# Kernel optimization log

Measured on AMD Instinct MI355X. Metric: run time of the kernel, lower is better.

The kernel has to match this reference:

```python
import jax, jax.numpy as jnp
import numpy as np

B, S, N, IN_DIM = 64, 12, 170, 1
E, L, C, H, OUT = 128, 4, 2, 8, 1
OFFSET, PAD = 0, 1          # seq_offset=0 -> Conv2d padding (0,1)
LOOKUP, MAXLEN = 0, 100
EPS = 1e-5


def _shift(x, s):
    """y[:, i] = x[:, i+s] along axis 1, zero padded."""
    if s == 0:
        return x
    z = jnp.zeros_like(x[:, :abs(s)])
    if s > 0:
        return jnp.concatenate([x[:, s:], z], axis=1)
    return jnp.concatenate([z, x[:, :s]], axis=1)


def _masked_conv_diag(x, w):
    """Diagonal of Conv2d(kernel=(1,3), pad=(0,PAD)) applied to the causally
    masked repeated tensor, computed directly without the O(B*S*S*E) blowup:
      out[b,i] = sum_k W[:,:,k] @ (mask(i, i+k-PAD) * x[b, i+k-PAD])
    where mask(i,j) = (j <= i) or (j < OFFSET)."""
    i = jnp.arange(x.shape[1])
    out = None
    for k in range(3):
        s = k - PAD
        term = jnp.einsum('bse,oe->bso', _shift(x, s), w[:, :, k])
        if s > 0:  # only future taps can be masked out
            term = term * (i + s < OFFSET).astype(x.dtype)[None, :, None]
        out = term if out is None else out + term
    return out


def _conv1d_k3(x, w, b):
    """Conv1d over the seq dim, kernel 3, padding 1, with bias. x:[b,s,e]."""
    out = b
    for k in range(3):
        out = out + jnp.einsum('bse,oe->bso', _shift(x, k - 1), w[:, :, k])
    return out


def _layer_norm(x, g, b):
    m = jnp.mean(x, -1, keepdims=True)
    v = jnp.mean((x - m) ** 2, -1, keepdims=True)
    return (x - m) * jax.lax.rsqrt(v + EPS) * g + b


def _mha(q_in, kv_in, w, b, mask=None):
    dh = E // H
    q = (q_in @ w[0] + b[0]).reshape(q_in.shape[0], q_in.shape[1], H, dh)
    k = (kv_in @ w[1] + b[1]).reshape(kv_in.shape[0], kv_in.shape[1], H, dh)
    v = (kv_in @ w[2] + b[2]).reshape(kv_in.shape[0], kv_in.shape[1], H, dh)
    s = jnp.einsum('bqhd,bkhd->bhqk', q, k) * np.float32(1.0 / np.sqrt(dh))
    if mask is not None:
        s = jnp.where(mask[None, None], s, jnp.float32(-1e9))
    a = jax.nn.softmax(s, axis=-1)
    o = jnp.einsum('bhqk,bkhd->bqhd', a, v).reshape(q_in.shape[0], q_in.shape[1], E)
    return o @ w[3] + b[3]


def setup_inputs() -> dict:
    key = jax.random.key(0)
    ks = jax.random.split(key, 16)

    def nrm(k, shape, scale=0.05):
        return scale * jax.random.normal(k, shape, dtype=jnp.float32)

    # sinusoidal positional table, length MAXLEN
    pos = np.arange(MAXLEN)[:, None].astype(np.float32)
    div = np.exp(-np.log(10000.0) * np.arange(0, E, 2) / E).astype(np.float32)
    pe = np.zeros((MAXLEN, E), np.float32)
    pe[:, 0::2] = np.sin(pos * div)
    pe[:, 1::2] = np.cos(pos * div)

    return {
        'x': jax.random.normal(ks[0], (B, S, N, IN_DIM), jnp.float32),
        'enc_x': jax.random.normal(ks[1], (C, B * N, S, E), jnp.float32),
        'tgt_mask': jnp.tril(jnp.ones((S, S), bool)),
        'emb_w': nrm(ks[2], (IN_DIM, E), 1.0),
        'emb_b': jnp.zeros((E,), jnp.float32),
        'pe': jnp.asarray(pe),
        'conv_q_w': nrm(ks[3], (L, E, E, 3)),
        'conv_k_w': nrm(ks[4], (L, C, E, E, 3)),
        'conv_k_b': jnp.zeros((L, C, E), jnp.float32),
        'sa_w': nrm(ks[5], (L, 4, E, E)),
        'sa_b': jnp.zeros((L, 4, E), jnp.float32),
        'ca_w': nrm(ks[6], (L, C, 4, E, E)),
        'ca_b': jnp.zeros((L, C, 4, E), jnp.float32),
        'ff_w1': nrm(ks[7], (L, E, 4 * E)),
        'ff_b1': jnp.zeros((L, 4 * E), jnp.float32),
        'ff_w2': nrm(ks[8], (L, 4 * E, E)),
        'ff_b2': jnp.zeros((L, E), jnp.float32),
        'ln_g': jnp.ones((L, 3, E), jnp.float32),
        'ln_b': jnp.zeros((L, 3, E), jnp.float32),
        'fc_w': nrm(ks[9], (E, OUT)),
        'fc_b': jnp.zeros((OUT,), jnp.float32),
    }


def reference(x, enc_x, tgt_mask, emb_w, emb_b, pe, conv_q_w, conv_k_w, conv_k_b,
              sa_w, sa_b, ca_w, ca_b, ff_w1, ff_b1, ff_w2, ff_b2, ln_g, ln_b,
              fc_w, fc_b):
    h = x @ emb_w + emb_b                                    # [B,S,N,E]
    h = jnp.transpose(h, (1, 0, 2, 3)).reshape(S, B * N, E)  # [S,B*N,E]
    h = jnp.transpose(h, (1, 0, 2))                          # [B*N,S,E]
    h = h + pe[LOOKUP:LOOKUP + S]
    for l in range(L):
        # local trends: causal masked-conv query (the fused diagonal)
        h = _masked_conv_diag(h, conv_q_w[l])
        enc_list = [_conv1d_k3(enc_x[i], conv_k_w[l, i], conv_k_b[l, i])
                    for i in range(C)]
        # decoder block: self-attn -> cross-attn (avg over features) -> FFN
        h = _layer_norm(h + _mha(h, h, sa_w[l], sa_b[l], tgt_mask),
                        ln_g[l, 0], ln_b[l, 0])
        cross = sum(_mha(h, enc_list[i], ca_w[l, i], ca_b[l, i])
                    for i in range(C)) / C
        h = _layer_norm(h + cross, ln_g[l, 1], ln_b[l, 1])
        f = jax.nn.relu(h @ ff_w1[l] + ff_b1[l]) @ ff_w2[l] + ff_b2[l]
        h = _layer_norm(h + f, ln_g[l, 2], ln_b[l, 2])
    out = h @ fc_w + fc_b                                    # [B*N,S,OUT]
    out = jnp.transpose(out, (1, 0, 2)).reshape(S, B, N, OUT)
    return jnp.transpose(out, (1, 0, 2, 3))                  # [B,S,N,OUT]
```

## Files before the change

kernel.cpp:

```cpp
#include <hip/hip_runtime.h>


#define B_   64
#define S_   12
#define N_   170
#define BN_  (B_*N_)
#define E_   128
#define L_   4
#define C_   2
#define H_   8
#define DH_  16
#define FF_  512
#define EPS_ 1e-5f
#define THREADS 512

typedef unsigned short u16;
typedef __attribute__((ext_vector_type(4))) float f32x4;
typedef __attribute__((ext_vector_type(8))) u16   us8;
typedef __attribute__((ext_vector_type(4))) u16   us4;
typedef __attribute__((ext_vector_type(8))) __bf16 bf16x8;
union FragU { us8 u; bf16x8 b; };

__device__ __forceinline__ u16 f2bf(float f) {
    __bf16 h = (__bf16)f;
    return __builtin_bit_cast(u16, h);
}
__device__ __forceinline__ float bf2f(u16 s) {
    return __builtin_bit_cast(float, (unsigned)s << 16);
}

__global__ void k_wpack(const float* __restrict__ cq, const float* __restrict__ sa,
                        const float* __restrict__ ck, const float* __restrict__ ca,
                        const float* __restrict__ f1, const float* __restrict__ f2,
                        u16* __restrict__ wp) {
    int f  = blockIdx.x * 256 + threadIdx.x;
    int l  = f / 57344, fl = f % 57344;
    const float* src; int sk, so, KS, q;
    if (fl < 4096)        { int tap = fl >> 11; q = fl & 2047; KS = 4;
                            src = cq + (size_t)l*49152 + tap;            sk = 3;   so = 384; }
    else if (fl < 12288)  { int j = (fl - 4096) >> 11; q = fl & 2047; KS = 4;
                            src = sa + (size_t)(l*4 + j)*16384;          sk = 128; so = 1;   }
    else if (fl < 24576)  { int ct = (fl - 12288) >> 11; q = fl & 2047; KS = 4;
                            int ci = ct / 3, tap = ct % 3;
                            src = ck + (size_t)(l*2 + ci)*49152 + tap;   sk = 3;   so = 384; }
    else if (fl < 40960)  { int cj = (fl - 24576) >> 11; q = fl & 2047; KS = 4;
                            src = ca + (size_t)(l*8 + cj)*16384;         sk = 128; so = 1;   }
    else if (fl < 49152)  { q = fl - 40960; KS = 4;
                            src = f1 + (size_t)l*65536;                  sk = 512; so = 1;   }
    else                  { q = fl - 49152; KS = 16;
                            src = f2 + (size_t)l*65536;                  sk = 128; so = 1;   }
    int lane = q & 63, tt = q >> 6;
    int ks = tt % KS, ntile = tt / KS;
    int k0 = ks*32 + ((lane >> 4) << 3);
    int o  = ntile*16 + (lane & 15);
    us8 w;
    #pragma unroll
    for (int i = 0; i < 8; i++) w[i] = f2bf(src[(size_t)(k0 + i)*sk + (size_t)o*so]);
    *(us8*)(wp + (size_t)f*8) = w;
}

__device__ __forceinline__ void stage48(const float* __restrict__ src, u16* dst, int t) {
    for (int i = t; i < 1536; i += THREADS) {
        const f32x4 v = ((const f32x4*)src)[i];
        int elem = i << 2;
        int row = elem >> 7, colb = (elem & 127) << 1;
        us4 w; w[0] = f2bf(v[0]); w[1] = f2bf(v[1]); w[2] = f2bf(v[2]); w[3] = f2bf(v[3]);
        *(us4*)((char*)dst + (((row << 8) + colb) ^ ((row & 7) << 4))) = w;
    }
}

__device__ __forceinline__ void stage48_embed(const float* __restrict__ x,
    const float* __restrict__ ew, const float* __restrict__ eb,
    const float* __restrict__ pe, int bn0, u16* dst, int t) {
    for (int i = t; i < 1536; i += THREADS) {
        int elem = i << 2;
        int row = elem >> 7, col = elem & 127;
        int g = row / 12, s = row - g*12;
        int bn = bn0 + g, b = bn / N_, n = bn - b*N_;
        float xv = x[(b*S_ + s)*N_ + n];
        const f32x4 w  = *(const f32x4*)(ew + col);
        const f32x4 bb = *(const f32x4*)(eb + col);
        const f32x4 p  = *(const f32x4*)(pe + s*E_ + col);
        us4 o; o[0] = f2bf(xv*w[0] + bb[0] + p[0]); o[1] = f2bf(xv*w[1] + bb[1] + p[1]);
               o[2] = f2bf(xv*w[2] + bb[2] + p[2]); o[3] = f2bf(xv*w[3] + bb[3] + p[3]);
        *(us4*)((char*)dst + (((row << 8) + (col << 1)) ^ ((row & 7) << 4))) = o;
    }
}

__device__ __forceinline__ void acc_init(f32x4 (&acc)[3], const float* bias, int wave, int lane) {
    float bv = bias ? bias[wave*16 + (lane & 15)] : 0.f;
    #pragma unroll
    for (int mt = 0; mt < 3; mt++) {
        acc[mt][0] = bv; acc[mt][1] = bv; acc[mt][2] = bv; acc[mt][3] = bv;
    }
}

__device__ __forceinline__ bf16x8 ldA(const u16* A, int row, int colb) {
    FragU fu; fu.u = *(const us8*)((const char*)A + (((row << 8) + colb) ^ ((row & 7) << 4)));
    return fu.b;
}

template<int KSTOT>
__device__ __forceinline__ void gemm48(const u16* A, const us8* __restrict__ WP, int ksOff,
                                       f32x4 (&acc)[3], int wave, int lane) {
    #pragma unroll
    for (int ks = 0; ks < 4; ks++) {
        int colb = (ks*32 + ((lane >> 4) << 3)) << 1;
        bf16x8 a[3];
        #pragma unroll
        for (int mt = 0; mt < 3; mt++) a[mt] = ldA(A, mt*16 + (lane & 15), colb);
        FragU fb; fb.u = WP[(wave*KSTOT + ksOff + ks)*64 + lane];
        #pragma unroll
        for (int mt = 0; mt < 3; mt++)
            acc[mt] = __builtin_amdgcn_mfma_f32_16x16x32_bf16(a[mt], fb.b, acc[mt], 0, 0, 0);
    }
}

__device__ __forceinline__ void gemm48_x3(const u16* A,
        const us8* __restrict__ B0, const us8* __restrict__ B1, const us8* __restrict__ B2,
        f32x4 (&c0)[3], f32x4 (&c1)[3], f32x4 (&c2)[3], int wave, int lane) {
    #pragma unroll
    for (int ks = 0; ks < 4; ks++) {
        int colb = (ks*32 + ((lane >> 4) << 3)) << 1;
        bf16x8 a[3];
        #pragma unroll
        for (int mt = 0; mt < 3; mt++) a[mt] = ldA(A, mt*16 + (lane & 15), colb);
        FragU f0, f1, f2;
        int bi = (wave*4 + ks)*64 + lane;
        f0.u = B0[bi]; f1.u = B1[bi]; f2.u = B2[bi];
        #pragma unroll
        for (int mt = 0; mt < 3; mt++) {
            c0[mt] = __builtin_amdgcn_mfma_f32_16x16x32_bf16(a[mt], f0.b, c0[mt], 0, 0, 0);
            c1[mt] = __builtin_amdgcn_mfma_f32_16x16x32_bf16(a[mt], f1.b, c1[mt], 0, 0, 0);
            c2[mt] = __builtin_amdgcn_mfma_f32_16x16x32_bf16(a[mt], f2.b, c2[mt], 0, 0, 0);
        }
    }
}

__device__ __forceinline__ void gemm48_x2(const u16* A,
        const us8* __restrict__ B0, const us8* __restrict__ B1,
        f32x4 (&c0)[3], f32x4 (&c1)[3], int wave, int lane) {
    #pragma unroll
    for (int ks = 0; ks < 4; ks++) {
        int colb = (ks*32 + ((lane >> 4) << 3)) << 1;
        bf16x8 a[3];
        #pragma unroll
        for (int mt = 0; mt < 3; mt++) a[mt] = ldA(A, mt*16 + (lane & 15), colb);
        FragU f0, f1;
        int bi = (wave*4 + ks)*64 + lane;
        f0.u = B0[bi]; f1.u = B1[bi];
        #pragma unroll
        for (int mt = 0; mt < 3; mt++) {
            c0[mt] = __builtin_amdgcn_mfma_f32_16x16x32_bf16(a[mt], f0.b, c0[mt], 0, 0, 0);
            c1[mt] = __builtin_amdgcn_mfma_f32_16x16x32_bf16(a[mt], f1.b, c1[mt], 0, 0, 0);
        }
    }
}

__device__ __forceinline__ void gemm48_rows(const u16* A, const u16* ZR, const int (&sr)[3],
                                            const us8* __restrict__ WP,
                                            f32x4 (&acc)[3], int wave, int lane) {
    #pragma unroll
    for (int ks = 0; ks < 4; ks++) {
        int colb = (ks*32 + ((lane >> 4) << 3)) << 1;
        bf16x8 a[3];
        #pragma unroll
        for (int mt = 0; mt < 3; mt++) {
            const char* p = (sr[mt] >= 0)
                ? (const char*)A + (((sr[mt] << 8) + colb) ^ ((sr[mt] & 7) << 4))
                : (const char*)ZR + colb;
            FragU fu; fu.u = *(const us8*)p;
            a[mt] = fu.b;
        }
        FragU fb; fb.u = WP[(wave*4 + ks)*64 + lane];
        #pragma unroll
        for (int mt = 0; mt < 3; mt++)
            acc[mt] = __builtin_amdgcn_mfma_f32_16x16x32_bf16(a[mt], fb.b, acc[mt], 0, 0, 0);
    }
}

template<bool RELU>
__device__ __forceinline__ void acc_store_bf(const f32x4 (&acc)[3], u16* Bp, int wave, int lane) {
    #pragma unroll
    for (int mt = 0; mt < 3; mt++)
    #pragma unroll
    for (int r = 0; r < 4; r++) {
        int row = mt*16 + ((lane >> 4) << 2) + r;
        int col = wave*16 + (lane & 15);
        float v = acc[mt][r];
        if (RELU) v = fmaxf(v, 0.f);
        *(u16*)((char*)Bp + (((row << 8) + (col << 1)) ^ ((row & 7) << 4))) = f2bf(v);
    }
}

__device__ __forceinline__ void ld16(const u16* Bf, int row, int colb, float* o16) {
    int x = (row & 7) << 4;
    int base = (row << 8) + colb;
    us8 u0 = *(const us8*)((const char*)Bf + (base ^ x));
    us8 u1 = *(const us8*)((const char*)Bf + ((base + 16) ^ x));
    #pragma unroll
    for (int d = 0; d < 8; d++) { o16[d] = bf2f(u0[d]); o16[8+d] = bf2f(u1[d]); }
}

template<bool MASK>
__device__ __forceinline__ void attn48(u16* QA, const u16* KB, const u16* VB, int t) {
    if (t < 384) {
        int g = t / 96, rem = t % 96;
        int hh = rem / 12, qi = rem % 12;
        int hb2 = hh << 5;
        int rq = g*12 + qi;
        float qv[16]; ld16(QA, rq, hb2, qv);
        float sc[12]; float mx = -1e30f;
        #pragma unroll
        for (int j = 0; j < 12; j++) {
            float kv[16]; ld16(KB, g*12 + j, hb2, kv);
            float s = 0.f;
            #pragma unroll
            for (int d = 0; d < 16; d++) s += qv[d]*kv[d];
            s *= 0.25f;
            if (MASK && j > qi) s = -1e30f;
            sc[j] = s; mx = fmaxf(mx, s);
        }
        float sum = 0.f;
        #pragma unroll
        for (int j = 0; j < 12; j++) { sc[j] = __expf(sc[j] - mx); sum += sc[j]; }
        float inv = 1.f/sum;
        float ov[16];
        #pragma unroll
        for (int d = 0; d < 16; d++) ov[d] = 0.f;
        #pragma unroll
        for (int j = 0; j < 12; j++) {
            float vv[16]; ld16(VB, g*12 + j, hb2, vv);
            #pragma unroll
            for (int d = 0; d < 16; d++) ov[d] += sc[j]*vv[d];
        }
        int x = (rq & 7) << 4;
        us8 w0, w1;
        #pragma unroll
        for (int d = 0; d < 8; d++) { w0[d] = f2bf(ov[d]*inv); w1[d] = f2bf(ov[8+d]*inv); }
        *(us8*)((char*)QA + (((rq << 8) + hb2) ^ x))      = w0;
        *(us8*)((char*)QA + (((rq << 8) + hb2 + 16) ^ x)) = w1;
    }
}

__device__ __forceinline__ void ln_inreg(f32x4 (&v)[3], float* lnbuf,
                                         const float* __restrict__ g, const float* __restrict__ bb,
                                         int wave, int lane) {
    int col = wave*16 + (lane & 15);
    float gc = g[col], bc = bb[col];
    #pragma unroll
    for (int mt = 0; mt < 3; mt++)
    #pragma unroll
    for (int r = 0; r < 4; r++) {
        float a = v[mt][r];
        float p = a, q = a*a;
        #pragma unroll
        for (int off = 1; off < 16; off <<= 1) { p += __shfl_xor(p, off); q += __shfl_xor(q, off); }
        if ((lane & 15) == 0) {
            int row = mt*16 + ((lane >> 4) << 2) + r;
            lnbuf[(row*8 + wave)*2]     = p;
            lnbuf[(row*8 + wave)*2 + 1] = q;
        }
    }
    __syncthreads();
    #pragma unroll
    for (int mt = 0; mt < 3; mt++)
    #pragma unroll
    for (int r = 0; r < 4; r++) {
        int row = mt*16 + ((lane >> 4) << 2) + r;
        float sum = 0.f, ss = 0.f;
        #pragma unroll
        for (int w2 = 0; w2 < 8; w2++) { sum += lnbuf[(row*8 + w2)*2]; ss += lnbuf[(row*8 + w2)*2 + 1]; }
        float m   = sum * (1.f/128.f);
        float var = ss * (1.f/128.f) - m*m;
        float inv = rsqrtf(var + EPS_);
        v[mt][r] = (v[mt][r] - m)*inv*gc + bc;
    }
}

template<bool EMB, bool FIN>
__global__ void __launch_bounds__(THREADS, 2)
k_layer(float* __restrict__ h, const float* __restrict__ x,
        const float* __restrict__ ew, const float* __restrict__ ebp, const float* __restrict__ pe,
        const float* __restrict__ encx, const u16* __restrict__ lw,
        const float* __restrict__ sab, const float* __restrict__ ckb, const float* __restrict__ cab,
        const float* __restrict__ fb1, const float* __restrict__ fb2,
        const float* __restrict__ lg, const float* __restrict__ lb,
        const float* __restrict__ fcw, const float* __restrict__ fcb,
        float* __restrict__ outp) {
    __shared__ __align__(16) u16 P0[6144], P1[6144], P2[6144], P3[6144], P4[6144], ZR[128];
    __shared__ __align__(16) float lnbuf[48*8*2];

    int t = threadIdx.x, wave = t >> 6, lane = t & 63;
    int bid = blockIdx.x;
    float* hp = h + (size_t)bid * (48*128);

    if (t < 64) ((unsigned*)ZR)[t] = 0;
    if (EMB) stage48_embed(x, ew, ebp, pe, bid*4, P0, t);
    else     stage48(hp, P0, t);
    stage48(encx + (size_t)(bid*4) * (S_*E_), P4, t);
    __syncthreads();

    int gg[3], rr[3];
    #pragma unroll
    for (int mt = 0; mt < 3; mt++) { int m = mt*16 + (lane & 15); gg[mt] = m/12; rr[mt] = m - gg[mt]*12; }

    f32x4 cacc[3];
    acc_init(cacc, nullptr, wave, lane);
    {
        int sr[3];
        #pragma unroll
        for (int mt = 0; mt < 3; mt++) { int r2 = rr[mt] - 1; sr[mt] = (r2 >= 0) ? gg[mt]*12 + r2 : -1; }
        gemm48_rows(P0, ZR, sr, (const us8*)lw, cacc, wave, lane);
        #pragma unroll
        for (int mt = 0; mt < 3; mt++) sr[mt] = gg[mt]*12 + rr[mt];
        gemm48_rows(P0, ZR, sr, (const us8*)(lw + 16384), cacc, wave, lane);
    }
    acc_store_bf<false>(cacc, P1, wave, lane);
    __syncthreads();

    {
        const us8* sap = (const us8*)(lw + 32768);
        f32x4 aq[3], ak[3], av[3];
        acc_init(aq, sab,       wave, lane);
        acc_init(ak, sab + 128, wave, lane);
        acc_init(av, sab + 256, wave, lane);
        gemm48_x3(P1, sap, sap + 2048, sap + 4096, aq, ak, av, wave, lane);
        acc_store_bf<false>(aq, P0, wave, lane);
        acc_store_bf<false>(ak, P2, wave, lane);
        acc_store_bf<false>(av, P3, wave, lane);
    }
    __syncthreads();
    attn48<true>(P0, P2, P3, t);
    __syncthreads();

    f32x4 hres[3];
    {
        f32x4 a[3];
        acc_init(a, sab + 384, wave, lane);
        gemm48<4>(P0, (const us8*)(lw + 81920), 0, a, wave, lane);
        #pragma unroll
        for (int mt = 0; mt < 3; mt++) hres[mt] = a[mt] + cacc[mt];
    }
    ln_inreg(hres, lnbuf, lg, lb, wave, lane);
    acc_store_bf<false>(hres, P1, wave, lane);
    __syncthreads();

    f32x4 creg[3];
    {
        int col = wave*16 + (lane & 15);
        float bv = cab[3*128 + col] + cab[7*128 + col];
        #pragma unroll
        for (int mt = 0; mt < 3; mt++) { creg[mt][0]=bv; creg[mt][1]=bv; creg[mt][2]=bv; creg[mt][3]=bv; }
    }
    int srf[3], srp[3], srn[3];
    #pragma unroll
    for (int mt = 0; mt < 3; mt++) {
        int r2 = rr[mt] - 1; srp[mt] = (r2 >= 0) ? gg[mt]*12 + r2 : -1;
        srf[mt] = gg[mt]*12 + rr[mt];
        r2 = rr[mt] + 1;     srn[mt] = (r2 < 12) ? gg[mt]*12 + r2 : -1;
    }

    {
        const us8* ckp = (const us8*)(lw + 98304);
        f32x4 a[3];
        acc_init(a, ckb, wave, lane);
        gemm48_rows(P4, ZR, srp, ckp,        a, wave, lane);
        gemm48_rows(P4, ZR, srf, ckp + 2048, a, wave, lane);
        gemm48_rows(P4, ZR, srn, ckp + 4096, a, wave, lane);
        acc_store_bf<false>(a, P3, wave, lane);
    }
    __syncthreads();
    const us8* cap0 = (const us8*)(lw + 196608);
    {
        f32x4 aq[3], ak[3], av[3];
        acc_init(aq, cab,           wave, lane);
        gemm48<4>(P1, cap0, 0, aq, wave, lane);
        acc_store_bf<false>(aq, P0, wave, lane);
        acc_init(ak, cab + 128, wave, lane);
        acc_init(av, cab + 256, wave, lane);
        gemm48_x2(P3, cap0 + 2048, cap0 + 4096, ak, av, wave, lane);
        acc_store_bf<false>(ak, P2, wave, lane);
        acc_store_bf<false>(av, P4, wave, lane);
    }
    __syncthreads();
    stage48(encx + ((size_t)BN_ + bid*4) * (S_*E_), P3, t);
    attn48<false>(P0, P2, P4, t);
    __syncthreads();
    gemm48<4>(P0, cap0 + 6144, 0, creg, wave, lane);
    __syncthreads();

    {
        const us8* ckp = (const us8*)(lw + 98304 + 3*16384);
        f32x4 a[3];
        acc_init(a, ckb + 128, wave, lane);
        gemm48_rows(P3, ZR, srp, ckp,        a, wave, lane);
        gemm48_rows(P3, ZR, srf, ckp + 2048, a, wave, lane);
        gemm48_rows(P3, ZR, srn, ckp + 4096, a, wave, lane);
        acc_store_bf<false>(a, P0, wave, lane);
    }
    __syncthreads();
    const us8* cap1 = (const us8*)(lw + 196608 + 4*16384);
    {
        f32x4 aq[3], ak[3], av[3];
        acc_init(aq, cab + 4*128, wave, lane);
        gemm48<4>(P1, cap1, 0, aq, wave, lane);
        acc_store_bf<false>(aq, P2, wave, lane);
        acc_init(ak, cab + 5*128, wave, lane);
        acc_init(av, cab + 6*128, wave, lane);
        gemm48_x2(P0, cap1 + 2048, cap1 + 4096, ak, av, wave, lane);
        acc_store_bf<false>(ak, P3, wave, lane);
        acc_store_bf<false>(av, P4, wave, lane);
    }
    __syncthreads();
    attn48<false>(P2, P3, P4, t);
    __syncthreads();
    gemm48<4>(P2, cap1 + 6144, 0, creg, wave, lane);

    #pragma unroll
    for (int mt = 0; mt < 3; mt++) hres[mt] = hres[mt] + 0.5f*creg[mt];
    __syncthreads();
    ln_inreg(hres, lnbuf, lg + 128, lb + 128, wave, lane);
    acc_store_bf<false>(hres, P1, wave, lane);
    __syncthreads();

    f32x4 ffacc[3];
    acc_init(ffacc, fb2, wave, lane);
    #pragma unroll
    for (int c = 0; c < 4; c++) {
        u16* MB = (c & 1) ? P3 : P2;
        {
            f32x4 a[3];
            acc_init(a, fb1 + c*128, wave, lane);
            gemm48<4>(P1, (const us8*)(lw + 327680) + c*2048, 0, a, wave, lane);
            acc_store_bf<true>(a, MB, wave, lane);
        }
        __syncthreads();
        gemm48<16>(MB, (const us8*)(lw + 393216), c*4, ffacc, wave, lane);
    }
    #pragma unroll
    for (int mt = 0; mt < 3; mt++) hres[mt] = hres[mt] + ffacc[mt];
    ln_inreg(hres, lnbuf, lg + 256, lb + 256, wave, lane);

    if (FIN) {
        float fw = fcw[wave*16 + (lane & 15)];
        float pr[3][4];
        #pragma unroll
        for (int mt = 0; mt < 3; mt++)
        #pragma unroll
        for (int r = 0; r < 4; r++) {
            float p = hres[mt][r]*fw;
            #pragma unroll
            for (int off = 1; off < 16; off <<= 1) p += __shfl_xor(p, off);
            pr[mt][r] = p;
        }
        __syncthreads();
        if ((lane & 15) == 0) {
            #pragma unroll
            for (int mt = 0; mt < 3; mt++)
            #pragma unroll
            for (int r = 0; r < 4; r++) {
                int row = mt*16 + ((lane >> 4) << 2) + r;
                lnbuf[row*8 + wave] = pr[mt][r];
            }
        }
        __syncthreads();
        if (t < 48) {
            float s8 = fcb[0];
            #pragma unroll
            for (int w2 = 0; w2 < 8; w2++) s8 += lnbuf[t*8 + w2];
            int bn = bid*4 + t/12, s = t % 12;
            int b = bn / N_, n = bn - b*N_;
            outp[(b*S_ + s)*N_ + n] = s8;
        }
    } else {
        #pragma unroll
        for (int mt = 0; mt < 3; mt++)
        #pragma unroll
        for (int r = 0; r < 4; r++) {
            int row = mt*16 + ((lane >> 4) << 2) + r;
            int col = wave*16 + (lane & 15);
            hp[row*128 + col] = hres[mt][r];
        }
    }
}

extern "C" void kernel_launch(void* const* d_in, const int* in_sizes, int n_in,
                              void* d_out, int out_size, void* d_ws, size_t ws_size,
                              hipStream_t stream) {
    const float* x        = (const float*)d_in[0];
    const float* enc_x    = (const float*)d_in[1];
    const float* emb_w    = (const float*)d_in[3];
    const float* emb_b    = (const float*)d_in[4];
    const float* pe       = (const float*)d_in[5];
    const float* conv_q_w = (const float*)d_in[6];
    const float* conv_k_w = (const float*)d_in[7];
    const float* conv_k_b = (const float*)d_in[8];
    const float* sa_w     = (const float*)d_in[9];
    const float* sa_b     = (const float*)d_in[10];
    const float* ca_w     = (const float*)d_in[11];
    const float* ca_b     = (const float*)d_in[12];
    const float* ff_w1    = (const float*)d_in[13];
    const float* ff_b1    = (const float*)d_in[14];
    const float* ff_w2    = (const float*)d_in[15];
    const float* ff_b2    = (const float*)d_in[16];
    const float* ln_g     = (const float*)d_in[17];
    const float* ln_b     = (const float*)d_in[18];
    const float* fc_w     = (const float*)d_in[19];
    const float* fc_b     = (const float*)d_in[20];

    const size_t HN = (size_t)BN_ * S_ * E_;
    float* h  = (float*)d_ws;
    u16* wpk  = (u16*)((float*)d_ws + HN);

    k_wpack<<<896, 256, 0, stream>>>(conv_q_w, sa_w, conv_k_w, ca_w, ff_w1, ff_w2, wpk);

    for (int l = 0; l < L_; l++) {
        const u16* lw = wpk + (size_t)l*458752;
        const float* sab = sa_b + l*512;
        const float* ckb = conv_k_b + l*256;
        const float* cab = ca_b + l*1024;
        const float* fb1 = ff_b1 + l*512;
        const float* fb2 = ff_b2 + l*128;
        const float* lg  = ln_g + l*384;
        const float* lb  = ln_b + l*384;
        if (l == 0)
            k_layer<true, false><<<BN_/4, THREADS, 0, stream>>>(h, x, emb_w, emb_b, pe, enc_x, lw,
                sab, ckb, cab, fb1, fb2, lg, lb, fc_w, fc_b, (float*)d_out);
        else if (l == L_-1)
            k_layer<false, true><<<BN_/4, THREADS, 0, stream>>>(h, x, emb_w, emb_b, pe, enc_x, lw,
                sab, ckb, cab, fb1, fb2, lg, lb, fc_w, fc_b, (float*)d_out);
        else
            k_layer<false, false><<<BN_/4, THREADS, 0, stream>>>(h, x, emb_w, emb_b, pe, enc_x, lw,
                sab, ckb, cab, fb1, fb2, lg, lb, fc_w, fc_b, (float*)d_out);
    }
}
```

Baseline: 1.832 ms.

## Shrink per-block tile to two sequences with padded 16-row groups and 2x2 wave tiles

Each block now handles 2 sequences (24 rows) instead of 4 (48 rows), using 256 threads. Each sequence is padded to 16 rows so every MFMA M-tile lines up with one sequence, and each wave computes a 2x2 block of 16x16 tiles instead of a 3x1 strip. The intent is to cut shared memory per block, raise occupancy, reuse each weight fragment across two M-tiles and simplify the conv row indexing. In exchange, 4 of every 16 rows are padding, so a quarter of the MFMA work is spent on unused rows, and each weight fragment is reused across fewer rows.

```diff
diff --git a/kernel.cpp b/kernel.cpp
--- a/kernel.cpp
+++ b/kernel.cpp
@@ -12,7 +12,7 @@
 #define DH_  16
 #define FF_  512
 #define EPS_ 1e-5f
-#define THREADS 512
+#define THREADS 256
 
 typedef unsigned short u16;
 typedef __attribute__((ext_vector_type(4))) float f32x4;
@@ -59,23 +59,32 @@
     *(us8*)(wp + (size_t)f*8) = w;
 }
 
-__device__ __forceinline__ void stage48(const float* __restrict__ src, u16* dst, int t) {
-    for (int i = t; i < 1536; i += THREADS) {
+__device__ __forceinline__ void stage24(const float* __restrict__ src, u16* dst, int t) {
+    #pragma unroll
+    for (int it = 0; it < 3; it++) {
+        int i = t + it*THREADS;
         const f32x4 v = ((const f32x4*)src)[i];
         int elem = i << 2;
-        int row = elem >> 7, colb = (elem & 127) << 1;
+        int srow = elem >> 7;
+        int g = srow / 12, s = srow - g*12;
+        int row = g*16 + s;
+        int colb = (elem & 127) << 1;
         us4 w; w[0] = f2bf(v[0]); w[1] = f2bf(v[1]); w[2] = f2bf(v[2]); w[3] = f2bf(v[3]);
         *(us4*)((char*)dst + (((row << 8) + colb) ^ ((row & 7) << 4))) = w;
     }
 }
 
-__device__ __forceinline__ void stage48_embed(const float* __restrict__ x,
+__device__ __forceinline__ void stage24_embed(const float* __restrict__ x,
     const float* __restrict__ ew, const float* __restrict__ eb,
     const float* __restrict__ pe, int bn0, u16* dst, int t) {
-    for (int i = t; i < 1536; i += THREADS) {
+    #pragma unroll
+    for (int it = 0; it < 3; it++) {
+        int i = t + it*THREADS;
         int elem = i << 2;
-        int row = elem >> 7, col = elem & 127;
-        int g = row / 12, s = row - g*12;
+        int srow = elem >> 7;
+        int g = srow / 12, s = srow - g*12;
+        int row = g*16 + s;
+        int col = elem & 127;
         int bn = bn0 + g, b = bn / N_, n = bn - b*N_;
         float xv = x[(b*S_ + s)*N_ + n];
         const f32x4 w  = *(const f32x4*)(ew + col);
@@ -87,11 +96,14 @@
     }
 }
 
-__device__ __forceinline__ void acc_init(f32x4 (&acc)[3], const float* bias, int wave, int lane) {
-    float bv = bias ? bias[wave*16 + (lane & 15)] : 0.f;
-    #pragma unroll
-    for (int mt = 0; mt < 3; mt++) {
-        acc[mt][0] = bv; acc[mt][1] = bv; acc[mt][2] = bv; acc[mt][3] = bv;
+__device__ __forceinline__ void acc_init(f32x4 (&acc)[2][2], const float* bias, int wave, int lane) {
+    #pragma unroll
+    for (int nt = 0; nt < 2; nt++) {
+        float bv = bias ? bias[(wave*2 + nt)*16 + (lane & 15)] : 0.f;
+        #pragma unroll
+        for (int mt = 0; mt < 2; mt++) {
+            acc[mt][nt][0] = bv; acc[mt][nt][1] = bv; acc[mt][nt][2] = bv; acc[mt][nt][3] = bv;
+        }
     }
 }
 
@@ -101,93 +113,105 @@
 }
 
 template<int KSTOT>
-__device__ __forceinline__ void gemm48(const u16* A, const us8* __restrict__ WP, int ksOff,
-                                       f32x4 (&acc)[3], int wave, int lane) {
+__device__ __forceinline__ void gemm24(const u16* A, const us8* __restrict__ WP, int ksOff,
+                                       f32x4 (&acc)[2][2], int wave, int lane) {
     #pragma unroll
     for (int ks = 0; ks < 4; ks++) {
         int colb = (ks*32 + ((lane >> 4) << 3)) << 1;
-        bf16x8 a[3];
-        #pragma unroll
-        for (int mt = 0; mt < 3; mt++) a[mt] = ldA(A, mt*16 + (lane & 15), colb);
-        FragU fb; fb.u = WP[(wave*KSTOT + ksOff + ks)*64 + lane];
-        #pragma unroll
-        for (int mt = 0; mt < 3; mt++)
-            acc[mt] = __builtin_amdgcn_mfma_f32_16x16x32_bf16(a[mt], fb.b, acc[mt], 0, 0, 0);
-    }
-}
-
-__device__ __forceinline__ void gemm48_x3(const u16* A,
-        const us8* __restrict__ B0, const us8* __restrict__ B1, const us8* __restrict__ B2,
-        f32x4 (&c0)[3], f32x4 (&c1)[3], f32x4 (&c2)[3], int wave, int lane) {
+        bf16x8 a[2];
+        #pragma unroll
+        for (int mt = 0; mt < 2; mt++) a[mt] = ldA(A, mt*16 + (lane & 15), colb);
+        #pragma unroll
+        for (int nt = 0; nt < 2; nt++) {
+            FragU fb; fb.u = WP[((wave*2 + nt)*KSTOT + ksOff + ks)*64 + lane];
+            #pragma unroll
+            for (int mt = 0; mt < 2; mt++)
+                acc[mt][nt] = __builtin_amdgcn_mfma_f32_16x16x32_bf16(a[mt], fb.b, acc[mt][nt], 0, 0, 0);
+        }
+    }
+}
+
+__device__ __forceinline__ void gemm24_rows(const u16* A, const u16* ZR, const int (&sr)[2],
+                                            const us8* __restrict__ WP,
+                                            f32x4 (&acc)[2][2], int wave, int lane) {
     #pragma unroll
     for (int ks = 0; ks < 4; ks++) {
         int colb = (ks*32 + ((lane >> 4) << 3)) << 1;
-        bf16x8 a[3];
-        #pragma unroll
-        for (int mt = 0; mt < 3; mt++) a[mt] = ldA(A, mt*16 + (lane & 15), colb);
-        FragU f0, f1, f2;
-        int bi = (wave*4 + ks)*64 + lane;
-        f0.u = B0[bi]; f1.u = B1[bi]; f2.u = B2[bi];
-        #pragma unroll
-        for (int mt = 0; mt < 3; mt++) {
-            c0[mt] = __builtin_amdgcn_mfma_f32_16x16x32_bf16(a[mt], f0.b, c0[mt], 0, 0, 0);
-            c1[mt] = __builtin_amdgcn_mfma_f32_16x16x32_bf16(a[mt], f1.b, c1[mt], 0, 0, 0);
-            c2[mt] = __builtin_amdgcn_mfma_f32_16x16x32_bf16(a[mt], f2.b, c2[mt], 0, 0, 0);
-        }
-    }
-}
-
-__device__ __forceinline__ void gemm48_x2(const u16* A,
-        const us8* __restrict__ B0, const us8* __restrict__ B1,
-        f32x4 (&c0)[3], f32x4 (&c1)[3], int wave, int lane) {
-    #pragma unroll
-    for (int ks = 0; ks < 4; ks++) {
-        int colb = (ks*32 + ((lane >> 4) << 3)) << 1;
-        bf16x8 a[3];
-        #pragma unroll
-        for (int mt = 0; mt < 3; mt++) a[mt] = ldA(A, mt*16 + (lane & 15), colb);
-        FragU f0, f1;
-        int bi = (wave*4 + ks)*64 + lane;
-        f0.u = B0[bi]; f1.u = B1[bi];
-        #pragma unroll
-        for (int mt = 0; mt < 3; mt++) {
-            c0[mt] = __builtin_amdgcn_mfma_f32_16x16x32_bf16(a[mt], f0.b, c0[mt], 0, 0, 0);
-            c1[mt] = __builtin_amdgcn_mfma_f32_16x16x32_bf16(a[mt], f1.b, c1[mt], 0, 0, 0);
-        }
-    }
-}
-
-__device__ __forceinline__ void gemm48_rows(const u16* A, const u16* ZR, const int (&sr)[3],
-                                            const us8* __restrict__ WP,
-                                            f32x4 (&acc)[3], int wave, int lane) {
-    #pragma unroll
-    for (int ks = 0; ks < 4; ks++) {
-        int colb = (ks*32 + ((lane >> 4) << 3)) << 1;
-        bf16x8 a[3];
-        #pragma unroll
-        for (int mt = 0; mt < 3; mt++) {
+        bf16x8 a[2];
+        #pragma unroll
+        for (int mt = 0; mt < 2; mt++) {
             const char* p = (sr[mt] >= 0)
                 ? (const char*)A + (((sr[mt] << 8) + colb) ^ ((sr[mt] & 7) << 4))
                 : (const char*)ZR + colb;
             FragU fu; fu.u = *(const us8*)p;
             a[mt] = fu.b;
         }
-        FragU fb; fb.u = WP[(wave*4 + ks)*64 + lane];
-        #pragma unroll
-        for (int mt = 0; mt < 3; mt++)
-            acc[mt] = __builtin_amdgcn_mfma_f32_16x16x32_bf16(a[mt], fb.b, acc[mt], 0, 0, 0);
+        #pragma unroll
+        for (int nt = 0; nt < 2; nt++) {
+            FragU fb; fb.u = WP[((wave*2 + nt)*4 + ks)*64 + lane];
+            #pragma unroll
+            for (int mt = 0; mt < 2; mt++)
+                acc[mt][nt] = __builtin_amdgcn_mfma_f32_16x16x32_bf16(a[mt], fb.b, acc[mt][nt], 0, 0, 0);
+        }
+    }
+}
+
+__device__ __forceinline__ void gemm24_x3(const u16* A,
+        const us8* __restrict__ B0, const us8* __restrict__ B1, const us8* __restrict__ B2,
+        f32x4 (&c0)[2][2], f32x4 (&c1)[2][2], f32x4 (&c2)[2][2], int wave, int lane) {
+    #pragma unroll
+    for (int ks = 0; ks < 4; ks++) {
+        int colb = (ks*32 + ((lane >> 4) << 3)) << 1;
+        bf16x8 a[2];
+        #pragma unroll
+        for (int mt = 0; mt < 2; mt++) a[mt] = ldA(A, mt*16 + (lane & 15), colb);
+        #pragma unroll
+        for (int nt = 0; nt < 2; nt++) {
+            int bi = ((wave*2 + nt)*4 + ks)*64 + lane;
+            FragU f0, f1, f2; f0.u = B0[bi]; f1.u = B1[bi]; f2.u = B2[bi];
+            #pragma unroll
+            for (int mt = 0; mt < 2; mt++) {
+                c0[mt][nt] = __builtin_amdgcn_mfma_f32_16x16x32_bf16(a[mt], f0.b, c0[mt][nt], 0, 0, 0);
+                c1[mt][nt] = __builtin_amdgcn_mfma_f32_16x16x32_bf16(a[mt], f1.b, c1[mt][nt], 0, 0, 0);
+                c2[mt][nt] = __builtin_amdgcn_mfma_f32_16x16x32_bf16(a[mt], f2.b, c2[mt][nt], 0, 0, 0);
+            }
+        }
+    }
+}
+
+__device__ __forceinline__ void gemm24_x2(const u16* A,
+        const us8* __restrict__ B0, const us8* __restrict__ B1,
+        f32x4 (&c0)[2][2], f32x4 (&c1)[2][2], int wave, int lane) {
+    #pragma unroll
+    for (int ks = 0; ks < 4; ks++) {
+        int colb = (ks*32 + ((lane >> 4) << 3)) << 1;
+        bf16x8 a[2];
+        #pragma unroll
+        for (int mt = 0; mt < 2; mt++) a[mt] = ldA(A, mt*16 + (lane & 15), colb);
+        #pragma unroll
+        for (int nt = 0; nt < 2; nt++) {
+            int bi = ((wave*2 + nt)*4 + ks)*64 + lane;
+            FragU f0, f1; f0.u = B0[bi]; f1.u = B1[bi];
+            #pragma unroll
+            for (int mt = 0; mt < 2; mt++) {
+                c0[mt][nt] = __builtin_amdgcn_mfma_f32_16x16x32_bf16(a[mt], f0.b, c0[mt][nt], 0, 0, 0);
+                c1[mt][nt] = __builtin_amdgcn_mfma_f32_16x16x32_bf16(a[mt], f1.b, c1[mt][nt], 0, 0, 0);
+            }
+        }
     }
 }
 
 template<bool RELU>
-__device__ __forceinline__ void acc_store_bf(const f32x4 (&acc)[3], u16* Bp, int wave, int lane) {
-    #pragma unroll
-    for (int mt = 0; mt < 3; mt++)
+__device__ __forceinline__ void acc_store_bf(const f32x4 (&acc)[2][2], u16* Bp, int wave, int lane) {
+    #pragma unroll
+    for (int mt = 0; mt < 2; mt++)
+    #pragma unroll
+    for (int nt = 0; nt < 2; nt++)
     #pragma unroll
     for (int r = 0; r < 4; r++) {
         int row = mt*16 + ((lane >> 4) << 2) + r;
-        int col = wave*16 + (lane & 15);
-        float v = acc[mt][r];
+        int col = (wave*2 + nt)*16 + (lane & 15);
+        float v = acc[mt][nt][r];
         if (RELU) v = fmaxf(v, 0.f);
         *(u16*)((char*)Bp + (((row << 8) + (col << 1)) ^ ((row & 7) << 4))) = f2bf(v);
     }
@@ -203,17 +227,17 @@
 }
 
 template<bool MASK>
-__device__ __forceinline__ void attn48(u16* QA, const u16* KB, const u16* VB, int t) {
-    if (t < 384) {
+__device__ __forceinline__ void attn24(u16* QA, const u16* KB, const u16* VB, int t) {
+    if (t < 192) {
         int g = t / 96, rem = t % 96;
         int hh = rem / 12, qi = rem % 12;
         int hb2 = hh << 5;
-        int rq = g*12 + qi;
+        int rq = g*16 + qi;
         float qv[16]; ld16(QA, rq, hb2, qv);
         float sc[12]; float mx = -1e30f;
         #pragma unroll
         for (int j = 0; j < 12; j++) {
-            float kv[16]; ld16(KB, g*12 + j, hb2, kv);
+            float kv[16]; ld16(KB, g*16 + j, hb2, kv);
             float s = 0.f;
             #pragma unroll
             for (int d = 0; d < 16; d++) s += qv[d]*kv[d];
@@ -230,7 +254,7 @@
         for (int d = 0; d < 16; d++) ov[d] = 0.f;
         #pragma unroll
         for (int j = 0; j < 12; j++) {
-            float vv[16]; ld16(VB, g*12 + j, hb2, vv);
+            float vv[16]; ld16(VB, g*16 + j, hb2, vv);
             #pragma unroll
             for (int d = 0; d < 16; d++) ov[d] += sc[j]*vv[d];
         }
@@ -243,38 +267,44 @@
     }
 }
 
-__device__ __forceinline__ void ln_inreg(f32x4 (&v)[3], float* lnbuf,
+__device__ __forceinline__ void ln_inreg(f32x4 (&v)[2][2], float* lnbuf,
                                          const float* __restrict__ g, const float* __restrict__ bb,
                                          int wave, int lane) {
-    int col = wave*16 + (lane & 15);
-    float gc = g[col], bc = bb[col];
-    #pragma unroll
-    for (int mt = 0; mt < 3; mt++)
+    float gc[2], bc[2];
+    #pragma unroll
+    for (int nt = 0; nt < 2; nt++) {
+        int col = (wave*2 + nt)*16 + (lane & 15);
+        gc[nt] = g[col]; bc[nt] = bb[col];
+    }
+    #pragma unroll
+    for (int mt = 0; mt < 2; mt++)
     #pragma unroll
     for (int r = 0; r < 4; r++) {
-        float a = v[mt][r];
-        float p = a, q = a*a;
+        float a = v[mt][0][r], c = v[mt][1][r];
+        float p = a + c, q = a*a + c*c;
         #pragma unroll
         for (int off = 1; off < 16; off <<= 1) { p += __shfl_xor(p, off); q += __shfl_xor(q, off); }
         if ((lane & 15) == 0) {
             int row = mt*16 + ((lane >> 4) << 2) + r;
-            lnbuf[(row*8 + wave)*2]     = p;
-            lnbuf[(row*8 + wave)*2 + 1] = q;
-        }
-    }
-    __syncthreads();
-    #pragma unroll
-    for (int mt = 0; mt < 3; mt++)
+            lnbuf[(row*4 + wave)*2]     = p;
+            lnbuf[(row*4 + wave)*2 + 1] = q;
+        }
+    }
+    __syncthreads();
+    #pragma unroll
+    for (int mt = 0; mt < 2; mt++)
     #pragma unroll
     for (int r = 0; r < 4; r++) {
         int row = mt*16 + ((lane >> 4) << 2) + r;
         float sum = 0.f, ss = 0.f;
         #pragma unroll
-        for (int w2 = 0; w2 < 8; w2++) { sum += lnbuf[(row*8 + w2)*2]; ss += lnbuf[(row*8 + w2)*2 + 1]; }
+        for (int w2 = 0; w2 < 4; w2++) { sum += lnbuf[(row*4 + w2)*2]; ss += lnbuf[(row*4 + w2)*2 + 1]; }
         float m   = sum * (1.f/128.f);
         float var = ss * (1.f/128.f) - m*m;
         float inv = rsqrtf(var + EPS_);
-        v[mt][r] = (v[mt][r] - m)*inv*gc + bc;
+        #pragma unroll
+        for (int nt = 0; nt < 2; nt++)
+            v[mt][nt][r] = (v[mt][nt][r] - m)*inv*gc[nt] + bc[nt];
     }
 }
 
@@ -288,168 +318,168 @@
         const float* __restrict__ lg, const float* __restrict__ lb,
         const float* __restrict__ fcw, const float* __restrict__ fcb,
         float* __restrict__ outp) {
-    __shared__ __align__(16) u16 P0[6144], P1[6144], P2[6144], P3[6144], P4[6144], ZR[128];
-    __shared__ __align__(16) float lnbuf[48*8*2];
+    __shared__ __align__(16) u16 P0[4096], P1[4096], P2[4096], P3[4096], P4[4096], ZR[128];
+    __shared__ __align__(16) float lnbuf[256];
 
     int t = threadIdx.x, wave = t >> 6, lane = t & 63;
     int bid = blockIdx.x;
-    float* hp = h + (size_t)bid * (48*128);
+    float* hp = h + (size_t)(bid*2) * (S_*E_);
 
     if (t < 64) ((unsigned*)ZR)[t] = 0;
-    if (EMB) stage48_embed(x, ew, ebp, pe, bid*4, P0, t);
-    else     stage48(hp, P0, t);
-    stage48(encx + (size_t)(bid*4) * (S_*E_), P4, t);
-    __syncthreads();
-
-    int gg[3], rr[3];
-    #pragma unroll
-    for (int mt = 0; mt < 3; mt++) { int m = mt*16 + (lane & 15); gg[mt] = m/12; rr[mt] = m - gg[mt]*12; }
-
-    f32x4 cacc[3];
+    if (EMB) stage24_embed(x, ew, ebp, pe, bid*2, P0, t);
+    else     stage24(hp, P0, t);
+    stage24(encx + (size_t)(bid*2) * (S_*E_), P4, t);
+    __syncthreads();
+
+    int rr = lane & 15;
+    int srp[2], srf[2], srn[2];
+    #pragma unroll
+    for (int mt = 0; mt < 2; mt++) {
+        srp[mt] = (rr >= 1)     ? mt*16 + rr - 1 : -1;
+        srf[mt] = mt*16 + rr;
+        srn[mt] = (rr + 1 < 12) ? mt*16 + rr + 1 : -1;
+    }
+
+    f32x4 cacc[2][2];
     acc_init(cacc, nullptr, wave, lane);
-    {
-        int sr[3];
-        #pragma unroll
-        for (int mt = 0; mt < 3; mt++) { int r2 = rr[mt] - 1; sr[mt] = (r2 >= 0) ? gg[mt]*12 + r2 : -1; }
-        gemm48_rows(P0, ZR, sr, (const us8*)lw, cacc, wave, lane);
-        #pragma unroll
-        for (int mt = 0; mt < 3; mt++) sr[mt] = gg[mt]*12 + rr[mt];
-        gemm48_rows(P0, ZR, sr, (const us8*)(lw + 16384), cacc, wave, lane);
-    }
+    gemm24_rows(P0, ZR, srp, (const us8*)lw,           cacc, wave, lane);
+    gemm24_rows(P0, ZR, srf, (const us8*)(lw + 16384), cacc, wave, lane);
     acc_store_bf<false>(cacc, P1, wave, lane);
     __syncthreads();
 
     {
         const us8* sap = (const us8*)(lw + 32768);
-        f32x4 aq[3], ak[3], av[3];
+        f32x4 aq[2][2], ak[2][2], av[2][2];
         acc_init(aq, sab,       wave, lane);
         acc_init(ak, sab + 128, wave, lane);
         acc_init(av, sab + 256, wave, lane);
-        gemm48_x3(P1, sap, sap + 2048, sap + 4096, aq, ak, av, wave, lane);
+        gemm24_x3(P1, sap, sap + 2048, sap + 4096, aq, ak, av, wave, lane);
         acc_store_bf<false>(aq, P0, wave, lane);
         acc_store_bf<false>(ak, P2, wave, lane);
         acc_store_bf<false>(av, P3, wave, lane);
     }
     __syncthreads();
-    attn48<true>(P0, P2, P3, t);
-    __syncthreads();
-
-    f32x4 hres[3];
+    attn24<true>(P0, P2, P3, t);
+    __syncthreads();
+
+    f32x4 hres[2][2];
     {
-        f32x4 a[3];
+        f32x4 a[2][2];
         acc_init(a, sab + 384, wave, lane);
-        gemm48<4>(P0, (const us8*)(lw + 81920), 0, a, wave, lane);
-        #pragma unroll
-        for (int mt = 0; mt < 3; mt++) hres[mt] = a[mt] + cacc[mt];
+        gemm24<4>(P0, (const us8*)(lw + 81920), 0, a, wave, lane);
+        #pragma unroll
+        for (int mt = 0; mt < 2; mt++)
+        #pragma unroll
+        for (int nt = 0; nt < 2; nt++) hres[mt][nt] = a[mt][nt] + cacc[mt][nt];
     }
     ln_inreg(hres, lnbuf, lg, lb, wave, lane);
     acc_store_bf<false>(hres, P1, wave, lane);
     __syncthreads();
 
-    f32x4 creg[3];
-    {
-        int col = wave*16 + (lane & 15);
+    f32x4 creg[2][2];
+    #pragma unroll
+    for (int nt = 0; nt < 2; nt++) {
+        int col = (wave*2 + nt)*16 + (lane & 15);
         float bv = cab[3*128 + col] + cab[7*128 + col];
         #pragma unroll
-        for (int mt = 0; mt < 3; mt++) { creg[mt][0]=bv; creg[mt][1]=bv; creg[mt][2]=bv; creg[mt][3]=bv; }
-    }
-    int srf[3], srp[3], srn[3];
-    #pragma unroll
-    for (int mt = 0; mt < 3; mt++) {
-        int r2 = rr[mt] - 1; srp[mt] = (r2 >= 0) ? gg[mt]*12 + r2 : -1;
-        srf[mt] = gg[mt]*12 + rr[mt];
-        r2 = rr[mt] + 1;     srn[mt] = (r2 < 12) ? gg[mt]*12 + r2 : -1;
+        for (int mt = 0; mt < 2; mt++) { creg[mt][nt][0]=bv; creg[mt][nt][1]=bv; creg[mt][nt][2]=bv; creg[mt][nt][3]=bv; }
     }
 
     {
         const us8* ckp = (const us8*)(lw + 98304);
-        f32x4 a[3];
+        f32x4 a[2][2];
         acc_init(a, ckb, wave, lane);
-        gemm48_rows(P4, ZR, srp, ckp,        a, wave, lane);
-        gemm48_rows(P4, ZR, srf, ckp + 2048, a, wave, lane);
-        gemm48_rows(P4, ZR, srn, ckp + 4096, a, wave, lane);
+        gemm24_rows(P4, ZR, srp, ckp,        a, wave, lane);
+        gemm24_rows(P4, ZR, srf, ckp + 2048, a, wave, lane);
+        gemm24_rows(P4, ZR, srn, ckp + 4096, a, wave, lane);
         acc_store_bf<false>(a, P3, wave, lane);
     }
     __syncthreads();
     const us8* cap0 = (const us8*)(lw + 196608);
     {
-        f32x4 aq[3], ak[3], av[3];
-        acc_init(aq, cab,           wave, lane);
-        gemm48<4>(P1, cap0, 0, aq, wave, lane);
+        f32x4 aq[2][2], ak[2][2], av[2][2];
+        acc_init(aq, cab, wave, lane);
+        gemm24<4>(P1, cap0, 0, aq, wave, lane);
         acc_store_bf<false>(aq, P0, wave, lane);
         acc_init(ak, cab + 128, wave, lane);
         acc_init(av, cab + 256, wave, lane);
-        gemm48_x2(P3, cap0 + 2048, cap0 + 4096, ak, av, wave, lane);
+        gemm24_x2(P3, cap0 + 2048, cap0 + 4096, ak, av, wave, lane);
         acc_store_bf<false>(ak, P2, wave, lane);
         acc_store_bf<false>(av, P4, wave, lane);
     }
     __syncthreads();
-    stage48(encx + ((size_t)BN_ + bid*4) * (S_*E_), P3, t);
-    attn48<false>(P0, P2, P4, t);
-    __syncthreads();
-    gemm48<4>(P0, cap0 + 6144, 0, creg, wave, lane);
+    stage24(encx + ((size_t)BN_ + bid*2) * (S_*E_), P3, t);
+    attn24<false>(P0, P2, P4, t);
+    __syncthreads();
+    gemm24<4>(P0, cap0 + 6144, 0, creg, wave, lane);
     __syncthreads();
 
     {
         const us8* ckp = (const us8*)(lw + 98304 + 3*16384);
-        f32x4 a[3];
+        f32x4 a[2][2];
         acc_init(a, ckb + 128, wave, lane);
-        gemm48_rows(P3, ZR, srp, ckp,        a, wave, lane);
-        gemm48_rows(P3, ZR, srf, ckp + 2048, a, wave, lane);
-        gemm48_rows(P3, ZR, srn, ckp + 4096, a, wave, lane);
+        gemm24_rows(P3, ZR, srp, ckp,        a, wave, lane);
+        gemm24_rows(P3, ZR, srf, ckp + 2048, a, wave, lane);
+        gemm24_rows(P3, ZR, srn, ckp + 4096, a, wave, lane);
         acc_store_bf<false>(a, P0, wave, lane);
     }
     __syncthreads();
     const us8* cap1 = (const us8*)(lw + 196608 + 4*16384);
     {
-        f32x4 aq[3], ak[3], av[3];
+        f32x4 aq[2][2], ak[2][2], av[2][2];
         acc_init(aq, cab + 4*128, wave, lane);
-        gemm48<4>(P1, cap1, 0, aq, wave, lane);
+        gemm24<4>(P1, cap1, 0, aq, wave, lane);
         acc_store_bf<false>(aq, P2, wave, lane);
         acc_init(ak, cab + 5*128, wave, lane);
         acc_init(av, cab + 6*128, wave, lane);
-        gemm48_x2(P0, cap1 + 2048, cap1 + 4096, ak, av, wave, lane);
+        gemm24_x2(P0, cap1 + 2048, cap1 + 4096, ak, av, wave, lane);
         acc_store_bf<false>(ak, P3, wave, lane);
         acc_store_bf<false>(av, P4, wave, lane);
     }
     __syncthreads();
-    attn48<false>(P2, P3, P4, t);
-    __syncthreads();
-    gemm48<4>(P2, cap1 + 6144, 0, creg, wave, lane);
-
-    #pragma unroll
-    for (int mt = 0; mt < 3; mt++) hres[mt] = hres[mt] + 0.5f*creg[mt];
+    attn24<false>(P2, P3, P4, t);
+    __syncthreads();
+    gemm24<4>(P2, cap1 + 6144, 0, creg, wave, lane);
+
+    #pragma unroll
+    for (int mt = 0; mt < 2; mt++)
+    #pragma unroll
+    for (int nt = 0; nt < 2; nt++) hres[mt][nt] = hres[mt][nt] + 0.5f*creg[mt][nt];
     __syncthreads();
     ln_inreg(hres, lnbuf, lg + 128, lb + 128, wave, lane);
     acc_store_bf<false>(hres, P1, wave, lane);
     __syncthreads();
 
-    f32x4 ffacc[3];
+    f32x4 ffacc[2][2];
     acc_init(ffacc, fb2, wave, lane);
     #pragma unroll
     for (int c = 0; c < 4; c++) {
         u16* MB = (c & 1) ? P3 : P2;
         {
-            f32x4 a[3];
+            f32x4 a[2][2];
             acc_init(a, fb1 + c*128, wave, lane);
-            gemm48<4>(P1, (const us8*)(lw + 327680) + c*2048, 0, a, wave, lane);
+            gemm24<4>(P1, (const us8*)(lw + 327680) + c*2048, 0, a, wave, lane);
             acc_store_bf<true>(a, MB, wave, lane);
         }
         __syncthreads();
-        gemm48<16>(MB, (const us8*)(lw + 393216), c*4, ffacc, wave, lane);
-    }
-    #pragma unroll
-    for (int mt = 0; mt < 3; mt++) hres[mt] = hres[mt] + ffacc[mt];
+        gemm24<16>(MB, (const us8*)(lw + 393216), c*4, ffacc, wave, lane);
+    }
+    #pragma unroll
+    for (int mt = 0; mt < 2; mt++)
+    #pragma unroll
+    for (int nt = 0; nt < 2; nt++) hres[mt][nt] = hres[mt][nt] + ffacc[mt][nt];
     ln_inreg(hres, lnbuf, lg + 256, lb + 256, wave, lane);
 
     if (FIN) {
-        float fw = fcw[wave*16 + (lane & 15)];
-        float pr[3][4];
-        #pragma unroll
-        for (int mt = 0; mt < 3; mt++)
+        float fw[2];
+        #pragma unroll
+        for (int nt = 0; nt < 2; nt++) fw[nt] = fcw[(wave*2 + nt)*16 + (lane & 15)];
+        float pr[2][4];
+        #pragma unroll
+        for (int mt = 0; mt < 2; mt++)
         #pragma unroll
         for (int r = 0; r < 4; r++) {
-            float p = hres[mt][r]*fw;
+            float p = hres[mt][0][r]*fw[0] + hres[mt][1][r]*fw[1];
             #pragma unroll
             for (int off = 1; off < 16; off <<= 1) p += __shfl_xor(p, off);
             pr[mt][r] = p;
@@ -457,30 +487,35 @@
         __syncthreads();
         if ((lane & 15) == 0) {
             #pragma unroll
-            for (int mt = 0; mt < 3; mt++)
+            for (int mt = 0; mt < 2; mt++)
             #pragma unroll
             for (int r = 0; r < 4; r++) {
                 int row = mt*16 + ((lane >> 4) << 2) + r;
-                lnbuf[row*8 + wave] = pr[mt][r];
+                lnbuf[row*4 + wave] = pr[mt][r];
             }
         }
         __syncthreads();
-        if (t < 48) {
-            float s8 = fcb[0];
-            #pragma unroll
-            for (int w2 = 0; w2 < 8; w2++) s8 += lnbuf[t*8 + w2];
-            int bn = bid*4 + t/12, s = t % 12;
+        if (t < 24) {
+            int g = t / 12, s = t % 12;
+            int row = g*16 + s;
+            float s4 = lnbuf[row*4] + lnbuf[row*4+1] + lnbuf[row*4+2] + lnbuf[row*4+3] + fcb[0];
+            int bn = bid*2 + g;
             int b = bn / N_, n = bn - b*N_;
-            outp[(b*S_ + s)*N_ + n] = s8;
+            outp[(b*S_ + s)*N_ + n] = s4;
         }
     } else {
         #pragma unroll
-        for (int mt = 0; mt < 3; mt++)
+        for (int mt = 0; mt < 2; mt++)
         #pragma unroll
         for (int r = 0; r < 4; r++) {
-            int row = mt*16 + ((lane >> 4) << 2) + r;
-            int col = wave*16 + (lane & 15);
-            hp[row*128 + col] = hres[mt][r];
+            int row = ((lane >> 4) << 2) + r;
+            if (row < 12) {
+                #pragma unroll
+                for (int nt = 0; nt < 2; nt++) {
+                    int col = (wave*2 + nt)*16 + (lane & 15);
+                    hp[(mt*S_ + row)*E_ + col] = hres[mt][nt][r];
+                }
+            }
         }
     }
 }
@@ -525,13 +560,13 @@
         const float* lg  = ln_g + l*384;
         const float* lb  = ln_b + l*384;
         if (l == 0)
-            k_layer<true, false><<<BN_/4, THREADS, 0, stream>>>(h, x, emb_w, emb_b, pe, enc_x, lw,
+            k_layer<true, false><<<BN_/2, THREADS, 0, stream>>>(h, x, emb_w, emb_b, pe, enc_x, lw,
                 sab, ckb, cab, fb1, fb2, lg, lb, fc_w, fc_b, (float*)d_out);
         else if (l == L_-1)
-            k_layer<false, true><<<BN_/4, THREADS, 0, stream>>>(h, x, emb_w, emb_b, pe, enc_x, lw,
+            k_layer<false, true><<<BN_/2, THREADS, 0, stream>>>(h, x, emb_w, emb_b, pe, enc_x, lw,
                 sab, ckb, cab, fb1, fb2, lg, lb, fc_w, fc_b, (float*)d_out);
         else
-            k_layer<false, false><<<BN_/4, THREADS, 0, stream>>>(h, x, emb_w, emb_b, pe, enc_x, lw,
+            k_layer<false, false><<<BN_/2, THREADS, 0, stream>>>(h, x, emb_w, emb_b, pe, enc_x, lw,
                 sab, ckb, cab, fb1, fb2, lg, lb, fc_w, fc_b, (float*)d_out);
     }
 }
```

New measurement: 1.546 ms. 1.18x faster.
